# Performance work log

Hardware: AMD Instinct MI355X
Metric: run time of the kernel (lower is better)

## Reference

```python
import jax, jax.numpy as jnp
import numpy as np

BETA = 0.25  # VectorQuantizer commitment beta


def setup_inputs() -> dict:
    key = jax.random.key(0)
    k1, k2, k3, k4 = jax.random.split(key, 4)
    B, T, Zc, D, K = 8, 4096, 512, 256, 8192
    x = jax.random.normal(k1, (B, T, 1, Zc), dtype=jnp.float32)
    W = jax.random.normal(k2, (Zc, D), dtype=jnp.float32) / np.sqrt(Zc)
    b = jax.random.normal(k3, (D,), dtype=jnp.float32) * 0.01
    codebook = jax.random.normal(k4, (K, D), dtype=jnp.float32) / np.sqrt(D)
    return {"x": x, "W": W, "b": b, "codebook": codebook}


def reference(x, W, b, codebook):
    sg = jax.lax.stop_gradient
    # quant_conv: Linear(z_channels -> embed_dim) after squeezing dim 2
    h = jnp.einsum('btc,cd->btd', jnp.squeeze(x, 2), W) + b  # [B,T,D]
    B, T, D = h.shape
    flat = h.reshape(-1, D)  # [B*T, D]
    # squared L2 distances to codebook: ||z||^2 + ||e||^2 - 2 z.e
    d = (jnp.sum(flat * flat, axis=1, keepdims=True)
         + jnp.sum(codebook * codebook, axis=1)
         - 2.0 * flat @ codebook.T)  # [B*T, K]
    idx = jnp.argmin(d, axis=1)  # [B*T]
    zq = jnp.take(codebook, idx, axis=0).reshape(B, T, D)
    # codebook + commitment loss
    emb_loss = (BETA * jnp.mean((sg(zq) - h) ** 2)
                + jnp.mean((zq - sg(h)) ** 2))
    # straight-through estimator
    zq = h + sg(zq - h)
    quant = zq[..., None]  # [B,T,D,1], matching h.unsqueeze(-1) layout
    return quant, emb_loss
```

## Files before the change

### kernel.cpp

```cpp
#include <hip/hip_runtime.h>
#include <stdint.h>

#define M_TOT 32768
#define ZC 512
#define DD 256
#define KCODES 8192
#define NGRAN 512
#define MARGIN 0.15f
#define NBUCKET 256

typedef _Float16 half8   __attribute__((ext_vector_type(8)));
typedef _Float16 half2v  __attribute__((ext_vector_type(2)));
typedef float    float4v __attribute__((ext_vector_type(4)));
typedef float    float16v __attribute__((ext_vector_type(16)));

#define OFF_H     0ull
#define OFF_HT    33554432ull
#define OFF_CBT   50331648ull
#define OFF_HH    54525952ull
#define OFF_EE    54657024ull
#define OFF_LOSSP 54689792ull
#define OFF_SMIN  54691840ull
#define OFF_WTH   OFF_SMIN
#define OFF_WTL   (OFF_SMIN + 524288ull)

#define ASYNC_CP16(gp, lp)                                                     \
  __builtin_amdgcn_global_load_lds(                                            \
      (const __attribute__((address_space(1))) void*)(gp),                     \
      (__attribute__((address_space(3))) void*)(lp), 16, 0, 0)

__global__ __launch_bounds__(256) void k_prep_w(const float* __restrict__ W,
                                                _Float16* __restrict__ wt_hi,
                                                _Float16* __restrict__ wt_lo) {
    const int idx = blockIdx.x * 256 + threadIdx.x;
    const int n = idx & 255, k = idx >> 8;
    const float v = W[(size_t)k * DD + n];
    const _Float16 hi = (_Float16)v;
    const _Float16 lo = (_Float16)(v - (float)hi);
    const int off = (((n >> 5) * 64 + (k >> 3)) << 8) + ((n & 31) << 3) + (k & 7);
    wt_hi[off] = hi;
    wt_lo[off] = lo;
}

__global__ __launch_bounds__(256) void k_gemm1(const float* __restrict__ x,
                                               const _Float16* __restrict__ wt_hi,
                                               const _Float16* __restrict__ wt_lo,
                                               const float* __restrict__ b,
                                               float* __restrict__ h) {
    __shared__ _Float16 sH[64 * 64];
    __shared__ _Float16 sL[64 * 64];
    const int tid = threadIdx.x, lane = tid & 63, w = tid >> 6;
    const int wy = w >> 1, wx = w & 1;
    const int m0 = blockIdx.x * 64;

    float16v acc[4];
#pragma unroll
    for (int j = 0; j < 4; ++j) acc[j] = (float16v)(0.0f);

    for (int kb = 0; kb < ZC; kb += 64) {
        __syncthreads();
        {
            const int m = tid & 63;
            const int kp = tid >> 6;
#pragma unroll
            for (int i2 = 0; i2 < 2; ++i2) {
                const int kg = kp * 2 + i2;
                const float* src = x + (size_t)(m0 + m) * ZC + kb + kg * 8;
                float4v v0 = *(const float4v*)src;
                float4v v1 = *(const float4v*)(src + 4);
                half8 hi, lo;
                float vv[8] = {v0.x, v0.y, v0.z, v0.w, v1.x, v1.y, v1.z, v1.w};
#pragma unroll
                for (int j = 0; j < 8; ++j) {
                    hi[j] = (_Float16)vv[j];
                    lo[j] = (_Float16)(vv[j] - (float)hi[j]);
                }
                const int off = (((m >> 5) * 8 + kg) << 8) + ((m & 31) << 3);
                *(half8*)&sH[off] = hi;
                *(half8*)&sL[off] = lo;
            }
        }
        __syncthreads();
#pragma unroll
        for (int s = 0; s < 4; ++s) {
            const int S = (kb >> 4) + s;
            half8 ah = *(const half8*)&sH[((wy * 8 + 2 * s) << 8) + lane * 8];
            half8 al = *(const half8*)&sL[((wy * 8 + 2 * s) << 8) + lane * 8];
#pragma unroll
            for (int nf = 0; nf < 4; ++nf) {
                const int nblk = wx * 4 + nf;
                const size_t boff = ((size_t)(nblk * 64 + 2 * S) << 8) + lane * 8;
                half8 bh = *(const half8*)&wt_hi[boff];
                half8 bl = *(const half8*)&wt_lo[boff];
                acc[nf] = __builtin_amdgcn_mfma_f32_32x32x16_f16(ah, bh, acc[nf], 0, 0, 0);
                acc[nf] = __builtin_amdgcn_mfma_f32_32x32x16_f16(ah, bl, acc[nf], 0, 0, 0);
                acc[nf] = __builtin_amdgcn_mfma_f32_32x32x16_f16(al, bh, acc[nf], 0, 0, 0);
            }
        }
    }
#pragma unroll
    for (int nf = 0; nf < 4; ++nf) {
        const int col = wx * 128 + nf * 32 + (lane & 31);
        const float bias = b[col];
#pragma unroll
        for (int r = 0; r < 16; ++r) {
            const int row = m0 + wy * 32 + (r & 3) + 8 * (r >> 2) + 4 * (lane >> 5);
            h[(size_t)row * DD + col] = acc[nf][r] + bias;
        }
    }
}

__global__ __launch_bounds__(256) void k_prep_h(const float* __restrict__ h,
                                                _Float16* __restrict__ ht,
                                                float* __restrict__ hh) {
    const int lane = threadIdx.x & 63, w = threadIdx.x >> 6;
    const int row = blockIdx.x * 4 + w;
    float4v v = *(const float4v*)&h[(size_t)row * DD + lane * 4];
    half2v p0, p1;
    p0.x = (_Float16)v.x; p0.y = (_Float16)v.y;
    p1.x = (_Float16)v.z; p1.y = (_Float16)v.w;
    const size_t off = ((size_t)((row >> 5) * 32 + (lane >> 1)) << 8) +
                       ((row & 31) << 3) + ((lane & 1) << 2);
    *(half2v*)&ht[off] = p0;
    *(half2v*)&ht[off + 2] = p1;
    float s = v.x * v.x + v.y * v.y + v.z * v.z + v.w * v.w;
#pragma unroll
    for (int o = 32; o; o >>= 1) s += __shfl_down(s, o);
    if (lane == 0) hh[row] = s;
}

__global__ __launch_bounds__(256) void k_prep_cb(const float* __restrict__ cb,
                                                 _Float16* __restrict__ cbt,
                                                 float* __restrict__ ee,
                                                 float* __restrict__ loss_part) {
    if (blockIdx.x == 0) loss_part[threadIdx.x] = 0.0f;
    const int lane = threadIdx.x & 63, w = threadIdx.x >> 6;
    const int code = blockIdx.x * 4 + w;
    float4v v = *(const float4v*)&cb[(size_t)code * DD + lane * 4];
    half2v p0, p1;
    p0.x = (_Float16)v.x; p0.y = (_Float16)v.y;
    p1.x = (_Float16)v.z; p1.y = (_Float16)v.w;
    const size_t off = ((size_t)((code >> 5) * 32 + (lane >> 1)) << 8) +
                       ((code & 31) << 3) + ((lane & 1) << 2);
    *(half2v*)&cbt[off] = p0;
    *(half2v*)&cbt[off + 2] = p1;
    float s = v.x * v.x + v.y * v.y + v.z * v.z + v.w * v.w;
#pragma unroll
    for (int o = 32; o; o >>= 1) s += __shfl_down(s, o);
    if (lane == 0) ee[code] = s;
}

__global__ __launch_bounds__(256, 2) void k_dist(const _Float16* __restrict__ ht,
                                                 const _Float16* __restrict__ cbt,
                                                 const float* __restrict__ ee,
                                                 _Float16* __restrict__ smin) {
    __shared__ _Float16 sB[128 * 256];
    const int tid = threadIdx.x, lane = tid & 63, w = tid >> 6;
    const int lw = lane & 31, csel = lane >> 5;
    const int bx = blockIdx.x;
    const int by = blockIdx.y;

    half8 afr[2][16];
    const size_t lo = (size_t)lane * 8;
#pragma unroll
    for (int mi = 0; mi < 2; ++mi) {
        const _Float16* base = cbt + (size_t)(bx * 8 + w * 2 + mi) * 8192;
#pragma unroll
        for (int s = 0; s < 16; ++s)
            afr[mi][s] = *(const half8*)(base + s * 512 + lo);
    }
    half8 aext[2], bext;
#pragma unroll
    for (int j = 0; j < 8; ++j) bext[j] = (_Float16)0.f;
    if (csel == 0) bext[0] = (_Float16)(-0.5f);
#pragma unroll
    for (int mi = 0; mi < 2; ++mi) {
        const float e = ee[bx * 256 + w * 64 + mi * 32 + lw];
#pragma unroll
        for (int j = 0; j < 8; ++j) aext[mi][j] = (_Float16)0.f;
        if (csel == 0) aext[mi][0] = (_Float16)e;
    }

    for (int it = 0; it < 8; ++it) {
        const int r0 = (by * 8 + it) * 128;
        __syncthreads();
        {
            const _Float16* g = ht + (size_t)r0 * 256 + w * 8192 + lane * 8;
            char* l = (char*)sB + w * 16384;
#pragma unroll
            for (int i = 0; i < 16; ++i)
                ASYNC_CP16(g + i * 512, l + i * 1024);
        }
        __syncthreads();

#pragma unroll 1
        for (int nj = 0; nj < 4; ++nj) {
            float16v acc0 = (float16v)(0.f), acc1 = (float16v)(0.f);
#pragma unroll
            for (int s = 0; s < 16; ++s) {
                half8 bf = *(const half8*)&sB[(size_t)((nj * 32 + 2 * s + csel) << 8) + lw * 8];
                acc0 = __builtin_amdgcn_mfma_f32_32x32x16_f16(afr[0][s], bf, acc0, 0, 0, 0);
                acc1 = __builtin_amdgcn_mfma_f32_32x32x16_f16(afr[1][s], bf, acc1, 0, 0, 0);
            }
            acc0 = __builtin_amdgcn_mfma_f32_32x32x16_f16(aext[0], bext, acc0, 0, 0, 0);
            acc1 = __builtin_amdgcn_mfma_f32_32x32x16_f16(aext[1], bext, acc1, 0, 0, 0);

            float g0a = acc0[0], g1a = acc0[8];
            float g0b = acc1[0], g1b = acc1[8];
#pragma unroll
            for (int r = 1; r < 8; ++r) {
                g0a = fmaxf(g0a, acc0[r]);  g1a = fmaxf(g1a, acc0[8 + r]);
                g0b = fmaxf(g0b, acc1[r]);  g1b = fmaxf(g1b, acc1[8 + r]);
            }
            g0a = fmaxf(g0a, __shfl_xor(g0a, 32));
            g1a = fmaxf(g1a, __shfl_xor(g1a, 32));
            g0b = fmaxf(g0b, __shfl_xor(g0b, 32));
            g1b = fmaxf(g1b, __shfl_xor(g1b, 32));
            if (lane < 32) {
                const int row = r0 + nj * 32 + lane;
                const int gb = bx * 16 + w * 4;
                smin[(size_t)(gb + 0) * M_TOT + row] = (_Float16)(-2.f * g0a);
                smin[(size_t)(gb + 1) * M_TOT + row] = (_Float16)(-2.f * g1a);
                smin[(size_t)(gb + 2) * M_TOT + row] = (_Float16)(-2.f * g0b);
                smin[(size_t)(gb + 3) * M_TOT + row] = (_Float16)(-2.f * g1b);
            }
        }
    }
}

__global__ __launch_bounds__(256, 2) void k_select(const float* __restrict__ h,
                                                   const float* __restrict__ cb,
                                                   const float* __restrict__ hh,
                                                   const float* __restrict__ ee,
                                                   const _Float16* __restrict__ smin,
                                                   float* __restrict__ out,
                                                   float* __restrict__ loss_part) {
    __shared__ _Float16 sS[64][512];
    const int t = threadIdx.x, lane = t & 63, w = t >> 6;
    const int r0 = blockIdx.x * 64;

    for (int gi = t; gi < NGRAN; gi += 256) {
        const _Float16* src = smin + (size_t)gi * M_TOT + r0;
#pragma unroll
        for (int c = 0; c < 8; ++c) {
            half8 v = *(const half8*)(src + c * 8);
#pragma unroll
            for (int j = 0; j < 8; ++j) sS[c * 8 + j][gi] = v[j];
        }
    }
    __syncthreads();

    float lossacc = 0.0f;
    for (int i = 0; i < 16; ++i) {
        const int row = r0 + w * 16 + i;
        float4v hv = *(const float4v*)&h[(size_t)row * DD + lane * 4];
        half8 sm = *(const half8*)&sS[w * 16 + i][lane * 8];
        float vmin = 1e30f;
        float sv[8];
#pragma unroll
        for (int j = 0; j < 8; ++j) {
            sv[j] = (float)sm[j];
            vmin = fminf(vmin, sv[j]);
        }
        float m2 = vmin;
#pragma unroll
        for (int o = 32; o; o >>= 1) m2 = fminf(m2, __shfl_xor(m2, o));
        const float thr = m2 + MARGIN;
        unsigned flags = 0;
#pragma unroll
        for (int j = 0; j < 8; ++j)
            if (sv[j] <= thr) flags |= (1u << j);

        unsigned long long act = __ballot(flags != 0);
        unsigned long long bestk = ~0ull;
        const float hhv = hh[row];
        while (act) {
            const int ln = __ffsll((long long)act) - 1;
            act &= act - 1;
            unsigned fl = (unsigned)__shfl((int)flags, ln);
            while (fl) {
                const int j = __ffs(fl) - 1;
                fl &= fl - 1;
                const int g = ln * 8 + j;
#pragma unroll
                for (int c = 0; c < 16; ++c) {
                    const int code = g * 16 + c;
                    float4v cv = *(const float4v*)&cb[(size_t)code * DD + lane * 4];
                    float s = hv.x * cv.x + hv.y * cv.y + hv.z * cv.z + hv.w * cv.w;
#pragma unroll
                    for (int o = 32; o; o >>= 1) s += __shfl_xor(s, o);
                    const float d = (hhv + ee[code]) - 2.0f * s;
                    const unsigned bts = __float_as_uint(d);
                    const unsigned mb =
                        bts ^ (unsigned)(((int)bts >> 31) | 0x80000000);
                    const unsigned long long key =
                        ((unsigned long long)mb << 32) | (unsigned)code;
                    if (key < bestk) bestk = key;
                }
            }
        }
        const unsigned best = (unsigned)(bestk & 0xffffffffull);
        float4v cv = *(const float4v*)&cb[(size_t)best * DD + lane * 4];
        *(float4v*)&out[(size_t)row * DD + lane * 4] = cv;
        const float dx = cv.x - hv.x, dy = cv.y - hv.y;
        const float dz = cv.z - hv.z, dw = cv.w - hv.w;
        lossacc += dx * dx + dy * dy + dz * dz + dw * dw;
    }
#pragma unroll
    for (int o = 32; o; o >>= 1) lossacc += __shfl_xor(lossacc, o);
    if (lane == 0)
        atomicAdd(&loss_part[(blockIdx.x * 4 + w) & (NBUCKET - 1)], lossacc);
}

__global__ __launch_bounds__(256) void k_final(const float* __restrict__ loss_part,
                                               float* __restrict__ out) {
    const int t = threadIdx.x;
    float s = loss_part[t];
#pragma unroll
    for (int off = 32; off; off >>= 1) s += __shfl_down(s, off);
    __shared__ float wsum[4];
    if ((t & 63) == 0) wsum[t >> 6] = s;
    __syncthreads();
    if (t == 0)
        out[0] = 1.25f * ((wsum[0] + wsum[1]) + (wsum[2] + wsum[3]))
                 / (float)(M_TOT * DD);
}

extern "C" void kernel_launch(void* const* d_in, const int* in_sizes, int n_in,
                              void* d_out, int out_size, void* d_ws, size_t ws_size,
                              hipStream_t stream) {
    const float* x  = (const float*)d_in[0];
    const float* W  = (const float*)d_in[1];
    const float* b  = (const float*)d_in[2];
    const float* cb = (const float*)d_in[3];
    float* out = (float*)d_out;

    char* ws = (char*)d_ws;
    float* h        = (float*)(ws + OFF_H);
    _Float16* ht    = (_Float16*)(ws + OFF_HT);
    _Float16* cbt   = (_Float16*)(ws + OFF_CBT);
    _Float16* wt_hi = (_Float16*)(ws + OFF_WTH);
    _Float16* wt_lo = (_Float16*)(ws + OFF_WTL);
    float* hh       = (float*)(ws + OFF_HH);
    float* ee       = (float*)(ws + OFF_EE);
    _Float16* smin  = (_Float16*)(ws + OFF_SMIN);
    float* loss_part = (float*)(ws + OFF_LOSSP);

    hipLaunchKernelGGL(k_prep_w, dim3(512), dim3(256), 0, stream, W, wt_hi, wt_lo);
    hipLaunchKernelGGL(k_prep_cb, dim3(KCODES / 4), dim3(256), 0, stream,
                       cb, cbt, ee, loss_part);
    hipLaunchKernelGGL(k_gemm1, dim3(M_TOT / 64), dim3(256), 0, stream,
                       x, wt_hi, wt_lo, b, h);
    hipLaunchKernelGGL(k_prep_h, dim3(M_TOT / 4), dim3(256), 0, stream,
                       h, ht, hh);
    hipLaunchKernelGGL(k_dist, dim3(KCODES / 256, M_TOT / 1024), dim3(256),
                       0, stream, ht, cbt, ee, smin);
    hipLaunchKernelGGL(k_select, dim3(M_TOT / 64), dim3(256), 0, stream,
                       h, cb, hh, ee, smin, out, loss_part);
    hipLaunchKernelGGL(k_final, dim3(1), dim3(256), 0, stream,
                       loss_part, out + (size_t)M_TOT * DD);
}
```

Before: 370.9 us.

## Double-buffer h tiles in k_dist to overlap async loads with MFMA

Splits the 128-row shared-memory tile of h into two 64-row buffers and prefetches the next tile with async copies while the current one is computed, waiting only on the older loads via vmcnt. It replaces the two __syncthreads per iteration with raw s_barrier calls and sched_barrier fences, and raises wave priority around the MFMA loop. The aim is to hide global-to-LDS load latency behind matrix math. The trade-off is more, smaller iterations and reliance on manual waitcnt correctness.

Result: no change. 374.2 us (+0.9%).

```diff
diff --git a/kernel.cpp b/kernel.cpp
--- a/kernel.cpp
+++ b/kernel.cpp
@@ -154,7 +154,7 @@
                                                  const _Float16* __restrict__ cbt,
                                                  const float* __restrict__ ee,
                                                  _Float16* __restrict__ smin) {
-    __shared__ _Float16 sB[128 * 256];
+    __shared__ _Float16 sB[2][64 * 256];
     const int tid = threadIdx.x, lane = tid & 63, w = tid >> 6;
     const int lw = lane & 31, csel = lane >> 5;
     const int bx = blockIdx.x;
@@ -181,51 +181,77 @@
         if (csel == 0) aext[mi][0] = (_Float16)e;
     }
 
-    for (int it = 0; it < 8; ++it) {
-        const int r0 = (by * 8 + it) * 128;
-        __syncthreads();
-        {
-            const _Float16* g = ht + (size_t)r0 * 256 + w * 8192 + lane * 8;
-            char* l = (char*)sB + w * 16384;
-#pragma unroll
-            for (int i = 0; i < 16; ++i)
-                ASYNC_CP16(g + i * 512, l + i * 1024);
-        }
-        __syncthreads();
+    const _Float16* hbase = ht + (size_t)by * 1024 * 256 + (size_t)w * 4096 + lane * 8;
+#define STAGE_HS(buf, t)                                                       \
+    do {                                                                       \
+        const _Float16* g_ = hbase + (size_t)(t) * 16384;                      \
+        char* l_ = (char*)&sB[(buf)][0] + w * 8192;                            \
+        _Pragma("unroll")                                                      \
+        for (int i_ = 0; i_ < 8; ++i_)                                         \
+            ASYNC_CP16(g_ + i_ * 512, l_ + i_ * 1024);                         \
+    } while (0)
+
+#define COMPUTE_HS(buf, t)                                                     \
+    do {                                                                       \
+        const int r0_ = by * 1024 + (t) * 64;                                  \
+        const _Float16* sb_ = &sB[(buf)][0];                                   \
+        _Pragma("unroll 1")                                                    \
+        for (int nj = 0; nj < 2; ++nj) {                                       \
+            float16v acc0 = (float16v)(0.f), acc1 = (float16v)(0.f);           \
+            __builtin_amdgcn_s_setprio(1);                                     \
+            _Pragma("unroll")                                                  \
+            for (int s = 0; s < 16; ++s) {                                     \
+                half8 bf = *(const half8*)&sb_[(size_t)((nj * 32 + 2 * s + csel) << 8) + lw * 8]; \
+                acc0 = __builtin_amdgcn_mfma_f32_32x32x16_f16(afr[0][s], bf, acc0, 0, 0, 0); \
+                acc1 = __builtin_amdgcn_mfma_f32_32x32x16_f16(afr[1][s], bf, acc1, 0, 0, 0); \
+            }                                                                  \
+            acc0 = __builtin_amdgcn_mfma_f32_32x32x16_f16(aext[0], bext, acc0, 0, 0, 0); \
+            acc1 = __builtin_amdgcn_mfma_f32_32x32x16_f16(aext[1], bext, acc1, 0, 0, 0); \
+            __builtin_amdgcn_s_setprio(0);                                     \
+             \
+             \
+            float g0a = acc0[0], g1a = acc0[8];                                \
+            float g0b = acc1[0], g1b = acc1[8];                                \
+            _Pragma("unroll")                                                  \
+            for (int r = 1; r < 8; ++r) {                                      \
+                g0a = fmaxf(g0a, acc0[r]);  g1a = fmaxf(g1a, acc0[8 + r]);     \
+                g0b = fmaxf(g0b, acc1[r]);  g1b = fmaxf(g1b, acc1[8 + r]);     \
+            }                                                                  \
+            g0a = fmaxf(g0a, __shfl_xor(g0a, 32));                             \
+            g1a = fmaxf(g1a, __shfl_xor(g1a, 32));                             \
+            g0b = fmaxf(g0b, __shfl_xor(g0b, 32));                             \
+            g1b = fmaxf(g1b, __shfl_xor(g1b, 32));                             \
+            if (lane < 32) {                                                   \
+                const int row_ = r0_ + nj * 32 + lane;                         \
+                const int gb_ = bx * 16 + w * 4;                               \
+                smin[(size_t)(gb_ + 0) * M_TOT + row_] = (_Float16)(-2.f * g0a); \
+                smin[(size_t)(gb_ + 1) * M_TOT + row_] = (_Float16)(-2.f * g1a); \
+                smin[(size_t)(gb_ + 2) * M_TOT + row_] = (_Float16)(-2.f * g0b); \
+                smin[(size_t)(gb_ + 3) * M_TOT + row_] = (_Float16)(-2.f * g1b); \
+            }                                                                  \
+        }                                                                      \
+    } while (0)
+
+    STAGE_HS(0, 0);
 
 #pragma unroll 1
-        for (int nj = 0; nj < 4; ++nj) {
-            float16v acc0 = (float16v)(0.f), acc1 = (float16v)(0.f);
-#pragma unroll
-            for (int s = 0; s < 16; ++s) {
-                half8 bf = *(const half8*)&sB[(size_t)((nj * 32 + 2 * s + csel) << 8) + lw * 8];
-                acc0 = __builtin_amdgcn_mfma_f32_32x32x16_f16(afr[0][s], bf, acc0, 0, 0, 0);
-                acc1 = __builtin_amdgcn_mfma_f32_32x32x16_f16(afr[1][s], bf, acc1, 0, 0, 0);
-            }
-            acc0 = __builtin_amdgcn_mfma_f32_32x32x16_f16(aext[0], bext, acc0, 0, 0, 0);
-            acc1 = __builtin_amdgcn_mfma_f32_32x32x16_f16(aext[1], bext, acc1, 0, 0, 0);
-
-            float g0a = acc0[0], g1a = acc0[8];
-            float g0b = acc1[0], g1b = acc1[8];
-#pragma unroll
-            for (int r = 1; r < 8; ++r) {
-                g0a = fmaxf(g0a, acc0[r]);  g1a = fmaxf(g1a, acc0[8 + r]);
-                g0b = fmaxf(g0b, acc1[r]);  g1b = fmaxf(g1b, acc1[8 + r]);
-            }
-            g0a = fmaxf(g0a, __shfl_xor(g0a, 32));
-            g1a = fmaxf(g1a, __shfl_xor(g1a, 32));
-            g0b = fmaxf(g0b, __shfl_xor(g0b, 32));
-            g1b = fmaxf(g1b, __shfl_xor(g1b, 32));
-            if (lane < 32) {
-                const int row = r0 + nj * 32 + lane;
-                const int gb = bx * 16 + w * 4;
-                smin[(size_t)(gb + 0) * M_TOT + row] = (_Float16)(-2.f * g0a);
-                smin[(size_t)(gb + 1) * M_TOT + row] = (_Float16)(-2.f * g1a);
-                smin[(size_t)(gb + 2) * M_TOT + row] = (_Float16)(-2.f * g0b);
-                smin[(size_t)(gb + 3) * M_TOT + row] = (_Float16)(-2.f * g1b);
-            }
-        }
-    }
+    for (int t = 0; t < 15; ++t) {
+        const int cur = t & 1;
+        STAGE_HS(cur ^ 1, t + 1);
+        asm volatile("s_waitcnt vmcnt(8)" ::: "memory");
+        __builtin_amdgcn_s_barrier();
+        __builtin_amdgcn_sched_barrier(0);
+        COMPUTE_HS(cur, t);
+        __builtin_amdgcn_sched_barrier(0);
+        __builtin_amdgcn_s_barrier();
+    }
+    asm volatile("s_waitcnt vmcnt(0)" ::: "memory");
+    __builtin_amdgcn_s_barrier();
+    __builtin_amdgcn_sched_barrier(0);
+    COMPUTE_HS(1, 15);
+
+#undef STAGE_HS
+#undef COMPUTE_HS
 }
 
 __global__ __launch_bounds__(256, 2) void k_select(const float* __restrict__ h,
```
